# Optimization experiments

Hardware: AMD Instinct MI355X
Metric: run time of the kernel (lower is better)

## Reference

```python
import jax, jax.numpy as jnp
import numpy as np

IN_DIM = 768
OUT_DIM = 4096
N_SK_ITER = 3
TARGET_TEMP = 0.06
PRED_TEMP = 0.12
PREFACTOR = 1.0
EXP_MAX = 50.0  # exp_max_values[float32]
SK_EPS = 1e-8
NORM_EPS = 1e-7


def setup_inputs() -> dict:
    key = jax.random.key(0)
    kx, kw = jax.random.split(key)
    x = jax.random.normal(kx, (16, 1024, IN_DIM), dtype=jnp.float32)
    # nn.Linear weight init: normal(std=1); bias zeros
    weight = jax.random.normal(kw, (OUT_DIM, IN_DIM), dtype=jnp.float32)
    bias = jnp.zeros((OUT_DIM,), dtype=jnp.float32)
    return {"x": x, "weight": weight, "bias": bias}


def sinkhorn_knopp(M, n_iterations, eps=SK_EPS):
    # stable_exp: shift by max over dim=-2 (token axis), add EXP_MAX
    shift = jnp.max(M, axis=-2, keepdims=True)
    M = jnp.exp(M + EXP_MAX - shift)
    for _ in range(n_iterations):  # small fixed count
        M = M / (jnp.sum(M, axis=-2, keepdims=True) + eps)  # column normalize
        M = M / (jnp.sum(M, axis=-1, keepdims=True) + eps)  # row normalize
    return M


def reference(x, weight, bias):
    # L2 normalize features (eps matches torch F.normalize with p=2)
    norm = jnp.maximum(jnp.linalg.norm(x, axis=-1, keepdims=True), NORM_EPS)
    x_n = x / norm
    logits = jnp.einsum("bnd,kd->bnk", x_n, weight) + bias  # [B, N, K]
    # positionwise_sk=True: no flatten before sinkhorn; detach -> stop_gradient
    assignments = sinkhorn_knopp(jax.lax.stop_gradient(logits) / TARGET_TEMP, N_SK_ITER)
    tgt = assignments.reshape(-1, OUT_DIM).astype(jnp.float32)
    pred = logits.reshape(-1, OUT_DIM).astype(jnp.float32)
    loss = -jnp.mean(jnp.sum(tgt * jax.nn.log_softmax(pred / PRED_TEMP, axis=-1), axis=-1))
    return assignments, PREFACTOR * loss
```

## Files before the change

kernel.cpp:

```cpp
#include <hip/hip_runtime.h>
#include <math.h>

#define BATCH 16
#define NTOK  1024
#define NCLU  4096
#define DIM   768
#define MROWS (BATCH * NTOK)

constexpr float TT_INV    = 16.666666666666668f;
constexpr float PT_INV    = 8.333333333333334f;
constexpr float SK_EPS_   = 1e-8f;
constexpr float NORM_EPS_ = 1e-7f;
constexpr float COL_SHIFT = 60.0f;
constexpr float P_SHIFT   = 40.0f;

typedef _Float16 f16x8 __attribute__((ext_vector_type(8)));
typedef _Float16 f16x4 __attribute__((ext_vector_type(4)));
typedef float    f32x4 __attribute__((ext_vector_type(4)));

struct F8 { float v[8]; };

__device__ __forceinline__ F8 load8(const float* p) {
    const float4 a = *(const float4*)p;
    const float4 b = *(const float4*)(p + 4);
    return F8{{a.x, a.y, a.z, a.w, b.x, b.y, b.z, b.w}};
}
__device__ __forceinline__ F8 load8(const _Float16* p) {
    f16x8 h = *(const f16x8*)p;
    F8 r;
#pragma unroll
    for (int i = 0; i < 8; ++i) r.v[i] = (float)h[i];
    return r;
}

__device__ __forceinline__ float wave_sum(float s) {
#pragma unroll
    for (int off = 32; off; off >>= 1) s += __shfl_xor(s, off);
    return s;
}

__device__ __forceinline__ void gl_lds16(const void* g, void* l) {
    __builtin_amdgcn_global_load_lds(
        (const __attribute__((address_space(1))) unsigned int*)g,
        (__attribute__((address_space(3))) unsigned int*)l,
        16, 0, 0);
}

__global__ __launch_bounds__(256) void castx_kernel(
    const float* __restrict__ x, _Float16* __restrict__ x16)
{
    int row  = (blockIdx.x * 256 + threadIdx.x) >> 6;
    int lane = threadIdx.x & 63;
    const float4* rp = (const float4*)(x + (size_t)row * DIM);
    float4 v[3];
    float ss = 0.f;
#pragma unroll
    for (int i = 0; i < 3; ++i) {
        v[i] = rp[lane + i * 64];
        ss += v[i].x * v[i].x + v[i].y * v[i].y + v[i].z * v[i].z + v[i].w * v[i].w;
    }
    ss = wave_sum(ss);
    float sc = 1.0f / fmaxf(sqrtf(ss), NORM_EPS_);
    _Float16* op = x16 + (size_t)row * DIM;
#pragma unroll
    for (int i = 0; i < 3; ++i) {
        f16x4 h;
        h[0] = (_Float16)(v[i].x * sc); h[1] = (_Float16)(v[i].y * sc);
        h[2] = (_Float16)(v[i].z * sc); h[3] = (_Float16)(v[i].w * sc);
        *(f16x4*)(op + 4 * (lane + i * 64)) = h;
    }
}

__global__ __launch_bounds__(256) void castw_kernel(
    const float* __restrict__ w, _Float16* __restrict__ w16)
{
    int i = blockIdx.x * 256 + threadIdx.x;
    const float4 a = *(const float4*)(w + (size_t)i * 8);
    const float4 b = *(const float4*)(w + (size_t)i * 8 + 4);
    f16x8 h;
    h[0] = (_Float16)a.x; h[1] = (_Float16)a.y; h[2] = (_Float16)a.z; h[3] = (_Float16)a.w;
    h[4] = (_Float16)b.x; h[5] = (_Float16)b.y; h[6] = (_Float16)b.z; h[7] = (_Float16)b.w;
    *(f16x8*)(w16 + (size_t)i * 8) = h;
}

__global__ __launch_bounds__(256) void rownorm_kernel(
    const float* __restrict__ x, float* __restrict__ invn)
{
    int wave = (blockIdx.x * 256 + threadIdx.x) >> 6;
    int lane = threadIdx.x & 63;
    const float4* row = (const float4*)(x + (size_t)wave * DIM);
    float s = 0.f;
#pragma unroll
    for (int i = 0; i < 3; ++i) {
        float4 v = row[lane + i * 64];
        s += v.x * v.x + v.y * v.y + v.z * v.z + v.w * v.w;
    }
    s = wave_sum(s);
    if (lane == 0) invn[wave] = 1.0f / fmaxf(sqrtf(s), NORM_EPS_);
}

#define BM 128
#define BN 128
#define BK 32

__global__ __launch_bounds__(256) void gemm16(
    const _Float16* __restrict__ A,
    const _Float16* __restrict__ B,
    const float* __restrict__ bias,
    _Float16* __restrict__ out,
    float* __restrict__ colpart)
{
    __shared__ __align__(16) _Float16 sh[2 * BM * BK];
    _Float16* As = sh;
    _Float16* Bs = sh + BM * BK;

    const int tid  = threadIdx.x;
    const int lane = tid & 63;
    const int wid  = tid >> 6;
    const int wr = wid >> 1, wc = wid & 1;

    const int nwg = gridDim.x;
    const int cpx = nwg >> 3;
    const int bid = blockIdx.x;
    const int swz = (bid & 7) * cpx + (bid >> 3);
    const int brow = (swz >> 5) * BM;
    const int bcol = (swz & 31) * BN;

    const int r  = lane >> 2;
    const int s4 = lane & 3;
    const int srcslot = s4 ^ (r & 3) ^ (r >> 2);
    const int c0 = wid * 2, c1 = wid * 2 + 1;

    const _Float16* gA0 = A + (size_t)(brow + c0 * 16 + r) * DIM + srcslot * 8;
    const _Float16* gA1 = A + (size_t)(brow + c1 * 16 + r) * DIM + srcslot * 8;
    const _Float16* gB0 = B + (size_t)(bcol + c0 * 16 + r) * DIM + srcslot * 8;
    const _Float16* gB1 = B + (size_t)(bcol + c1 * 16 + r) * DIM + srcslot * 8;
    _Float16* lA0 = &As[c0 * 16 * BK];
    _Float16* lA1 = &As[c1 * 16 * BK];
    _Float16* lB0 = &Bs[c0 * 16 * BK];
    _Float16* lB1 = &Bs[c1 * 16 * BK];

    const int q  = lane >> 4;
    const int fr = lane & 15;
    const int slot = q ^ (fr & 3) ^ ((fr >> 2) & 3);
    const int aoff = (wr * 64 + fr) * BK + slot * 8;
    const int boff = (wc * 64 + fr) * BK + slot * 8;

    f32x4 acc[4][4] = {};

    const int NT = DIM / BK;
    for (int kt = 0; kt < NT; ++kt) {
        const int ko = kt * BK;
        __syncthreads();
        gl_lds16(gA0 + ko, lA0);
        gl_lds16(gA1 + ko, lA1);
        gl_lds16(gB0 + ko, lB0);
        gl_lds16(gB1 + ko, lB1);
        __syncthreads();

        f16x8 af[4], bf[4];
#pragma unroll
        for (int m = 0; m < 4; ++m)
            af[m] = *(const f16x8*)&As[aoff + m * 16 * BK];
#pragma unroll
        for (int n = 0; n < 4; ++n)
            bf[n] = *(const f16x8*)&Bs[boff + n * 16 * BK];
#pragma unroll
        for (int m = 0; m < 4; ++m)
#pragma unroll
            for (int n = 0; n < 4; ++n)
                acc[m][n] = __builtin_amdgcn_mfma_f32_16x16x32_f16(
                    af[m], bf[n], acc[m][n], 0, 0, 0);
    }

    float cs[4] = {0.f, 0.f, 0.f, 0.f};
    _Float16* Ct = sh;
#pragma unroll
    for (int h = 0; h < 2; ++h) {
        __syncthreads();
        if (wr == h) {
#pragma unroll
            for (int n = 0; n < 4; ++n) {
                const int coll = wc * 64 + n * 16 + fr;
                const float bv = bias[bcol + coll];
#pragma unroll
                for (int m = 0; m < 4; ++m) {
#pragma unroll
                    for (int j = 0; j < 4; ++j) {
                        float v = acc[m][n][j] + bv;
                        Ct[(m * 16 + (q << 2) + j) * BN + coll] = (_Float16)v;
                        cs[n] += __expf(v * TT_INV - COL_SHIFT);
                    }
                }
            }
        }
        __syncthreads();
#pragma unroll
        for (int i = 0; i < 4; ++i) {
            int c   = tid + i * 256;
            int rl  = c >> 4;
            int c16 = c & 15;
            f16x8 v = *(const f16x8*)&Ct[rl * BN + c16 * 8];
            *(f16x8*)(out + (size_t)(brow + h * 64 + rl) * NCLU + bcol + c16 * 8) = v;
        }
    }

    __syncthreads();
    float* cred = (float*)sh;
#pragma unroll
    for (int n = 0; n < 4; ++n) {
        float c2 = cs[n];
        c2 += __shfl_xor(c2, 16);
        c2 += __shfl_xor(c2, 32);
        if (q == 0) cred[((wr * 2 + wc) * 4 + n) * 16 + fr] = c2;
    }
    __syncthreads();
    if (tid < 128) {
        int wc2 = tid >> 6, n2 = (tid >> 4) & 3, fr2 = tid & 15;
        float S = cred[((0 * 2 + wc2) * 4 + n2) * 16 + fr2]
                + cred[((1 * 2 + wc2) * 4 + n2) * 16 + fr2];
        colpart[(size_t)(brow >> 7) * NCLU + bcol + wc2 * 64 + n2 * 16 + fr2] = S;
    }
}

__global__ __launch_bounds__(256) void colfin_kernel(
    const float* __restrict__ part, float* __restrict__ a1)
{
    int i = blockIdx.x * 256 + threadIdx.x;
    int b = i >> 12, k = i & (NCLU - 1);
    const float* p = part + (size_t)(b * 8) * NCLU + k;
    float s = 0.f;
#pragma unroll
    for (int rb = 0; rb < 8; ++rb) { s += *p; p += NCLU; }
    a1[i] = -COL_SHIFT - __logf(s);
}

#define LDK 40

__device__ __forceinline__ f16x8 pack8(float4 lo, float4 hi, float sc) {
    f16x8 h;
    h[0] = (_Float16)(lo.x * sc); h[1] = (_Float16)(lo.y * sc);
    h[2] = (_Float16)(lo.z * sc); h[3] = (_Float16)(lo.w * sc);
    h[4] = (_Float16)(hi.x * sc); h[5] = (_Float16)(hi.y * sc);
    h[6] = (_Float16)(hi.z * sc); h[7] = (_Float16)(hi.w * sc);
    return h;
}

template <typename OT>
__global__ __launch_bounds__(256) void gemm_f16(
    const float* __restrict__ x, const float* __restrict__ w,
    const float* __restrict__ bias, const float* __restrict__ invn,
    OT* __restrict__ out)
{
    __shared__ __align__(16) _Float16 As[BM * LDK];
    __shared__ __align__(16) _Float16 Bs[BN * LDK];

    const int tid  = threadIdx.x;
    const int lane = tid & 63;
    const int wid  = tid >> 6;
    const int wr = wid >> 1, wc = wid & 1;
    const int brow = blockIdx.y * BM;
    const int bcol = blockIdx.x * BN;

    const int r0 = tid >> 2;
    const int r1 = r0 + 64;
    const int kc = (tid & 3) * 8;
    const float sA0 = invn[brow + r0];
    const float sA1 = invn[brow + r1];
    const float* gA0 = x + (size_t)(brow + r0) * DIM + kc;
    const float* gA1 = x + (size_t)(brow + r1) * DIM + kc;
    const float* gB0 = w + (size_t)(bcol + r0) * DIM + kc;
    const float* gB1 = w + (size_t)(bcol + r1) * DIM + kc;

    f32x4 acc[4][4] = {};
    float4 a00, a01, a10, a11, b00, b01, b10, b11;
    a00 = *(const float4*)(gA0);     a01 = *(const float4*)(gA0 + 4);
    a10 = *(const float4*)(gA1);     a11 = *(const float4*)(gA1 + 4);
    b00 = *(const float4*)(gB0);     b01 = *(const float4*)(gB0 + 4);
    b10 = *(const float4*)(gB1);     b11 = *(const float4*)(gB1 + 4);

    const int NT = DIM / BK;
    for (int kt = 0; kt < NT; ++kt) {
        __syncthreads();
        *(f16x8*)&As[r0 * LDK + kc] = pack8(a00, a01, sA0);
        *(f16x8*)&As[r1 * LDK + kc] = pack8(a10, a11, sA1);
        *(f16x8*)&Bs[r0 * LDK + kc] = pack8(b00, b01, 1.0f);
        *(f16x8*)&Bs[r1 * LDK + kc] = pack8(b10, b11, 1.0f);
        __syncthreads();

        if (kt + 1 < NT) {
            int k0 = (kt + 1) * BK;
            a00 = *(const float4*)(gA0 + k0); a01 = *(const float4*)(gA0 + k0 + 4);
            a10 = *(const float4*)(gA1 + k0); a11 = *(const float4*)(gA1 + k0 + 4);
            b00 = *(const float4*)(gB0 + k0); b01 = *(const float4*)(gB0 + k0 + 4);
            b10 = *(const float4*)(gB1 + k0); b11 = *(const float4*)(gB1 + k0 + 4);
        }

        const int ko = (lane >> 4) * 8;
        f16x8 af[4], bf[4];
#pragma unroll
        for (int m = 0; m < 4; ++m)
            af[m] = *(const f16x8*)&As[(wr * 64 + m * 16 + (lane & 15)) * LDK + ko];
#pragma unroll
        for (int n = 0; n < 4; ++n)
            bf[n] = *(const f16x8*)&Bs[(wc * 64 + n * 16 + (lane & 15)) * LDK + ko];
#pragma unroll
        for (int m = 0; m < 4; ++m)
#pragma unroll
            for (int n = 0; n < 4; ++n)
                acc[m][n] = __builtin_amdgcn_mfma_f32_16x16x32_f16(
                    af[m], bf[n], acc[m][n], 0, 0, 0);
    }

#pragma unroll
    for (int n = 0; n < 4; ++n) {
        int col = bcol + wc * 64 + n * 16 + (lane & 15);
        float bv = bias[col];
#pragma unroll
        for (int m = 0; m < 4; ++m) {
            int row0 = brow + wr * 64 + m * 16 + ((lane >> 4) << 2);
#pragma unroll
            for (int j = 0; j < 4; ++j)
                out[(size_t)(row0 + j) * NCLU + col] = (OT)(acc[m][n][j] + bv);
        }
    }
}

template <typename T>
__global__ __launch_bounds__(256) void colpass_kernel(
    const T* __restrict__ L, const float* __restrict__ a_in,
    const float* __restrict__ b_in, float* __restrict__ a_out)
{
    __shared__ float bsh[NTOK];
    __shared__ float ss[4][64];
    int b = blockIdx.x >> 6;
    int k = ((blockIdx.x & 63) << 6) + (threadIdx.x & 63);
    int wv = threadIdx.x >> 6;
    int lane = threadIdx.x & 63;
    const bool first = (b_in == nullptr);
    if (first) {
        for (int i = threadIdx.x; i < NTOK; i += 256) bsh[i] = 0.f;
    } else {
        for (int i = threadIdx.x; i < NTOK; i += 256) bsh[i] = b_in[b * NTOK + i];
    }
    __syncthreads();
    float aval = first ? -COL_SHIFT : a_in[b * NCLU + k];
    const T* p = L + (size_t)b * NTOK * NCLU + (size_t)(wv * 256) * NCLU + k;
    float s = 0.f;
#pragma unroll 4
    for (int n = 0; n < 256; ++n) {
        s += __expf((float)(*p) * TT_INV + aval + bsh[wv * 256 + n]);
        p += NCLU;
    }
    ss[wv][lane] = s;
    __syncthreads();
    if (wv == 0) {
        float S = ss[0][lane] + ss[1][lane] + ss[2][lane] + ss[3][lane];
        a_out[b * NCLU + k] = aval - __logf(first ? S : S + SK_EPS_);
    }
}

template <typename T>
__global__ __launch_bounds__(256) void colpassV_kernel(
    const T* __restrict__ L, const float* __restrict__ a_in,
    const float* __restrict__ b_in, float* __restrict__ a_out)
{
    __shared__ float bsh[NTOK];
    __shared__ float red[16][16][8];
    const int b     = blockIdx.x >> 5;
    const int strip = blockIdx.x & 31;
    const int cc    = threadIdx.x & 15;
    const int rg    = threadIdx.x >> 4;
    const int col0  = strip * 128 + cc * 8;
    for (int i = threadIdx.x; i < NTOK; i += 256) bsh[i] = b_in[b * NTOK + i];
    __syncthreads();
    const float4 av0 = *(const float4*)(a_in + b * NCLU + col0);
    const float4 av1 = *(const float4*)(a_in + b * NCLU + col0 + 4);
    const float av[8] = {av0.x, av0.y, av0.z, av0.w, av1.x, av1.y, av1.z, av1.w};
    float s[8] = {};
    const T* p = L + (size_t)b * NTOK * NCLU + (size_t)rg * NCLU + col0;
    for (int it = 0; it < 64; ++it) {
        F8 Lv = load8(p);
        float bpv = bsh[it * 16 + rg];
#pragma unroll
        for (int j = 0; j < 8; ++j) s[j] += __expf(Lv.v[j] * TT_INV + av[j] + bpv);
        p += (size_t)16 * NCLU;
    }
#pragma unroll
    for (int j = 0; j < 8; ++j) red[rg][cc][j] = s[j];
    __syncthreads();
    if (threadIdx.x < 128) {
        int c2 = threadIdx.x >> 3, j2 = threadIdx.x & 7;
        float S = 0.f;
#pragma unroll
        for (int g = 0; g < 16; ++g) S += red[g][c2][j2];
        int col = strip * 128 + c2 * 8 + j2;
        a_out[b * NCLU + col] = a_in[b * NCLU + col] - __logf(S + SK_EPS_);
    }
}

template <typename T>
__global__ __launch_bounds__(256) void rowpass_kernel(
    const T* __restrict__ L, const float* __restrict__ a_in,
    const float* __restrict__ b_in, float* __restrict__ b_out)
{
    int row  = (blockIdx.x * 256 + threadIdx.x) >> 6;
    int lane = threadIdx.x & 63;
    int b = row >> 10;
    const T* Lr = L + (size_t)row * NCLU;
    const float* av = a_in + (size_t)b * NCLU;
    float bp = b_in ? b_in[row] : 0.f;
    float s = 0.f;
#pragma unroll
    for (int i = 0; i < 8; ++i) {
        int c = i * 64 + lane;
        F8 Lv = load8(Lr + c * 8);
        F8 Av = load8(av + c * 8);
#pragma unroll
        for (int j = 0; j < 8; ++j)
            s += __expf(Lv.v[j] * TT_INV + Av.v[j] + bp);
    }
    s = wave_sum(s);
    if (lane == 0) b_out[row] = bp - __logf(s + SK_EPS_);
}

template <typename T>
__global__ __launch_bounds__(256) void final_kernel(
    const T* __restrict__ L, const float* __restrict__ a3,
    const float* __restrict__ b2, float* __restrict__ out,
    float* __restrict__ rowloss)
{
    __shared__ float red[3][4];
    const int row  = blockIdx.x;
    const int tid  = threadIdx.x;
    const int lane = tid & 63;
    const int wv   = tid >> 6;
    const int b    = row >> 10;
    const T* Lr = L + (size_t)row * NCLU;
    const float* av = a3 + (size_t)b * NCLU;
    const float bp = b2[row];

    float e[2][8];
    float rs = 0.f, q = 0.f, sP = 0.f;
#pragma unroll
    for (int jj = 0; jj < 2; ++jj) {
        int c = tid + jj * 256;
        F8 Lv = load8(Lr + c * 8);
        F8 Av = load8(av + c * 8);
#pragma unroll
        for (int j = 0; j < 8; ++j) {
            float P  = Lv.v[j] * PT_INV;
            float ev = __expf(Lv.v[j] * TT_INV + Av.v[j] + bp);
            e[jj][j] = ev;
            rs += ev;
            q  += ev * P;
            sP += __expf(P - P_SHIFT);
        }
    }
    rs = wave_sum(rs); q = wave_sum(q); sP = wave_sum(sP);
    if (lane == 0) { red[0][wv] = rs; red[1][wv] = q; red[2][wv] = sP; }
    __syncthreads();
    rs = red[0][0] + red[0][1] + red[0][2] + red[0][3];
    q  = red[1][0] + red[1][1] + red[1][2] + red[1][3];
    sP = red[2][0] + red[2][1] + red[2][2] + red[2][3];

    const float inv = 1.0f / (rs + SK_EPS_);
    const float lse = P_SHIFT + __logf(sP);

    float* Or = out + (size_t)row * NCLU;
#pragma unroll
    for (int jj = 0; jj < 2; ++jj) {
        int c = tid + jj * 256;
        f32x4 w0, w1;
        w0[0] = e[jj][0] * inv; w0[1] = e[jj][1] * inv;
        w0[2] = e[jj][2] * inv; w0[3] = e[jj][3] * inv;
        w1[0] = e[jj][4] * inv; w1[1] = e[jj][5] * inv;
        w1[2] = e[jj][6] * inv; w1[3] = e[jj][7] * inv;
        __builtin_nontemporal_store(w0, (f32x4*)(Or + c * 8));
        __builtin_nontemporal_store(w1, (f32x4*)(Or + c * 8 + 4));
    }
    if (tid == 0) rowloss[row] = q * inv - lse * (rs * inv);
}

__global__ __launch_bounds__(256) void lossred_kernel(
    const float* __restrict__ rowloss, float* __restrict__ out_loss)
{
    __shared__ float red[4];
    int tid = threadIdx.x, lane = tid & 63, wv = tid >> 6;
    float s = 0.f;
    for (int i = tid; i < MROWS; i += 256) s += rowloss[i];
    s = wave_sum(s);
    if (lane == 0) red[wv] = s;
    __syncthreads();
    if (tid == 0)
        out_loss[0] = -(red[0] + red[1] + red[2] + red[3]) / (float)MROWS;
}

extern "C" void kernel_launch(void* const* d_in, const int* in_sizes, int n_in,
                              void* d_out, int out_size, void* d_ws, size_t ws_size,
                              hipStream_t stream)
{
    const float* x    = (const float*)d_in[0];
    const float* w    = (const float*)d_in[1];
    const float* bias = (const float*)d_in[2];
    float* out = (float*)d_out;
    char* base = (char*)d_ws;
    float* ws  = (float*)d_ws;

    float* a1      = ws;
    float* a2      = a1 + BATCH * NCLU;
    float* a3      = a2 + BATCH * NCLU;
    float* b1      = a3 + BATCH * NCLU;
    float* b2      = b1 + MROWS;
    float* rowloss = b2 + MROWS;

    const size_t SMALL = 1u << 20;
    const size_t L16B  = (size_t)MROWS * NCLU * 2;
    const size_t X16B  = (size_t)MROWS * DIM * 2;
    const size_t W16B  = (size_t)NCLU * DIM * 2;
    const size_t PARTB = (size_t)128 * NCLU * 4;

    const int CB = BATCH * (NCLU / 64);
    const int RB = MROWS / 4;

    if (ws_size >= SMALL + L16B + X16B + W16B + PARTB) {
        _Float16* L16 = (_Float16*)(base + SMALL);
        _Float16* X16 = (_Float16*)(base + SMALL + L16B);
        _Float16* W16 = (_Float16*)(base + SMALL + L16B + X16B);
        float*    part = (float*)(base + SMALL + L16B + X16B + W16B);
        castx_kernel<<<MROWS / 4, 256, 0, stream>>>(x, X16);
        castw_kernel<<<(NCLU * DIM / 8) / 256, 256, 0, stream>>>(w, W16);
        gemm16<<<(MROWS / BM) * (NCLU / BN), 256, 0, stream>>>(X16, W16, bias, L16, part);
        colfin_kernel<<<BATCH * NCLU / 256, 256, 0, stream>>>(part, a1);
        rowpass_kernel<_Float16><<<RB, 256, 0, stream>>>(L16, a1, nullptr, b1);
        colpassV_kernel<_Float16><<<BATCH * 32, 256, 0, stream>>>(L16, a1, b1, a2);
        rowpass_kernel<_Float16><<<RB, 256, 0, stream>>>(L16, a2, b1, b2);
        colpassV_kernel<_Float16><<<BATCH * 32, 256, 0, stream>>>(L16, a2, b2, a3);
        final_kernel<_Float16><<<MROWS, 256, 0, stream>>>(L16, a3, b2, out, rowloss);
        lossred_kernel<<<1, 256, 0, stream>>>(rowloss, out + (size_t)MROWS * NCLU);
    } else if (ws_size >= SMALL + L16B) {
        float* invn = rowloss + MROWS;
        _Float16* L16 = (_Float16*)(base + SMALL);
        rownorm_kernel<<<MROWS / 4, 256, 0, stream>>>(x, invn);
        dim3 gg(NCLU / BN, MROWS / BM);
        gemm_f16<_Float16><<<gg, 256, 0, stream>>>(x, w, bias, invn, L16);
        colpass_kernel<_Float16><<<CB, 256, 0, stream>>>(L16, nullptr, nullptr, a1);
        rowpass_kernel<_Float16><<<RB, 256, 0, stream>>>(L16, a1, nullptr, b1);
        colpassV_kernel<_Float16><<<BATCH * 32, 256, 0, stream>>>(L16, a1, b1, a2);
        rowpass_kernel<_Float16><<<RB, 256, 0, stream>>>(L16, a2, b1, b2);
        colpassV_kernel<_Float16><<<BATCH * 32, 256, 0, stream>>>(L16, a2, b2, a3);
        final_kernel<_Float16><<<MROWS, 256, 0, stream>>>(L16, a3, b2, out, rowloss);
        lossred_kernel<<<1, 256, 0, stream>>>(rowloss, out + (size_t)MROWS * NCLU);
    } else {
        float* invn = rowloss + MROWS;
        rownorm_kernel<<<MROWS / 4, 256, 0, stream>>>(x, invn);
        dim3 gg(NCLU / BN, MROWS / BM);
        gemm_f16<float><<<gg, 256, 0, stream>>>(x, w, bias, invn, out);
        colpass_kernel<float><<<CB, 256, 0, stream>>>(out, nullptr, nullptr, a1);
        rowpass_kernel<float><<<RB, 256, 0, stream>>>(out, a1, nullptr, b1);
        colpassV_kernel<float><<<BATCH * 32, 256, 0, stream>>>(out, a1, b1, a2);
        rowpass_kernel<float><<<RB, 256, 0, stream>>>(out, a2, b1, b2);
        colpassV_kernel<float><<<BATCH * 32, 256, 0, stream>>>(out, a2, b2, a3);
        final_kernel<float><<<MROWS, 256, 0, stream>>>(out, a3, b2, out, rowloss);
        lossred_kernel<<<1, 256, 0, stream>>>(rowloss, out + (size_t)MROWS * NCLU);
    }
}
```

Measured before the change: 375.8 us.

## Fuse Sinkhorn row and column passes into a single chunked kernel

Adds a kernel that, for each 16-row chunk, computes the row normalizers and then builds per-chunk column partial sums weighted by those normalizers. A small reduction kernel then finalizes the column scalings. This replaces the separate rowpass and colpassV launches and aims to cut full passes over the half-precision logits; the scratch space reuses the now-dead X16 region. The GEMM epilogue also drops its LDS-staged vectorized stores in favour of direct scattered 2-byte global stores, which saves barriers but may hurt write coalescing.

```diff
diff --git a/kernel.cpp b/kernel.cpp
--- a/kernel.cpp
+++ b/kernel.cpp
@@ -110,9 +110,8 @@
     _Float16* __restrict__ out,
     float* __restrict__ colpart)
 {
-    __shared__ __align__(16) _Float16 sh[2 * BM * BK];
-    _Float16* As = sh;
-    _Float16* Bs = sh + BM * BK;
+    __shared__ __align__(16) _Float16 As[BM * BK];
+    __shared__ __align__(16) _Float16 Bs[BN * BK];
 
     const int tid  = threadIdx.x;
     const int lane = tid & 63;
@@ -174,39 +173,23 @@
     }
 
     float cs[4] = {0.f, 0.f, 0.f, 0.f};
-    _Float16* Ct = sh;
-#pragma unroll
-    for (int h = 0; h < 2; ++h) {
-        __syncthreads();
-        if (wr == h) {
-#pragma unroll
-            for (int n = 0; n < 4; ++n) {
-                const int coll = wc * 64 + n * 16 + fr;
-                const float bv = bias[bcol + coll];
-#pragma unroll
-                for (int m = 0; m < 4; ++m) {
-#pragma unroll
-                    for (int j = 0; j < 4; ++j) {
-                        float v = acc[m][n][j] + bv;
-                        Ct[(m * 16 + (q << 2) + j) * BN + coll] = (_Float16)v;
-                        cs[n] += __expf(v * TT_INV - COL_SHIFT);
-                    }
-                }
+#pragma unroll
+    for (int n = 0; n < 4; ++n) {
+        int col = bcol + wc * 64 + n * 16 + fr;
+        float bv = bias[col];
+#pragma unroll
+        for (int m = 0; m < 4; ++m) {
+            int row0 = brow + wr * 64 + m * 16 + (q << 2);
+#pragma unroll
+            for (int j = 0; j < 4; ++j) {
+                float v = acc[m][n][j] + bv;
+                out[(size_t)(row0 + j) * NCLU + col] = (_Float16)v;
+                cs[n] += __expf(v * TT_INV - COL_SHIFT);
             }
         }
-        __syncthreads();
-#pragma unroll
-        for (int i = 0; i < 4; ++i) {
-            int c   = tid + i * 256;
-            int rl  = c >> 4;
-            int c16 = c & 15;
-            f16x8 v = *(const f16x8*)&Ct[rl * BN + c16 * 8];
-            *(f16x8*)(out + (size_t)(brow + h * 64 + rl) * NCLU + bcol + c16 * 8) = v;
-        }
-    }
-
-    __syncthreads();
-    float* cred = (float*)sh;
+    }
+    __syncthreads();
+    float* cred = (float*)&As[0];
 #pragma unroll
     for (int n = 0; n < 4; ++n) {
         float c2 = cs[n];
@@ -233,6 +216,94 @@
 #pragma unroll
     for (int rb = 0; rb < 8; ++rb) { s += *p; p += NCLU; }
     a1[i] = -COL_SHIFT - __logf(s);
+}
+
+template <bool FIRST>
+__global__ __launch_bounds__(256) void rcpass_kernel(
+    const _Float16* __restrict__ L, const float* __restrict__ a_in,
+    const float* __restrict__ b_in, float* __restrict__ b_out,
+    float* __restrict__ part)
+{
+    __shared__ float wgt_sh[16];
+    const int tid  = threadIdx.x;
+    const int lane = tid & 63;
+    const int wv   = tid >> 6;
+    const int chunk = blockIdx.x;
+    const int b     = chunk >> 6;
+    const int row0  = chunk * 16;
+    const float* av = a_in + (size_t)b * NCLU;
+
+    float ar[8][8];
+#pragma unroll
+    for (int i = 0; i < 8; ++i) {
+        int c = i * 64 + lane;
+        *(float4*)&ar[i][0] = *(const float4*)&av[c * 8];
+        *(float4*)&ar[i][4] = *(const float4*)&av[c * 8 + 4];
+    }
+
+#pragma unroll
+    for (int rr = 0; rr < 4; ++rr) {
+        int row = row0 + wv * 4 + rr;
+        const _Float16* Lr = L + (size_t)row * NCLU;
+        float bp = FIRST ? 0.f : b_in[row];
+        float s = 0.f;
+#pragma unroll
+        for (int i = 0; i < 8; ++i) {
+            int c = i * 64 + lane;
+            f16x8 h = *(const f16x8*)&Lr[c * 8];
+#pragma unroll
+            for (int j = 0; j < 8; ++j)
+                s += __expf((float)h[j] * TT_INV + ar[i][j] + bp);
+        }
+        s = wave_sum(s);
+        if (lane == 0) {
+            float bn = bp - __logf(s + SK_EPS_);
+            b_out[row] = bn;
+            wgt_sh[wv * 4 + rr] = __expf(bn);
+        }
+    }
+    __syncthreads();
+
+    float aown[2][8];
+#pragma unroll
+    for (int sl = 0; sl < 2; ++sl) {
+        *(float4*)&aown[sl][0] = *(const float4*)&av[sl * 2048 + tid * 8];
+        *(float4*)&aown[sl][4] = *(const float4*)&av[sl * 2048 + tid * 8 + 4];
+    }
+    float acc[2][8] = {};
+    for (int rr = 0; rr < 16; ++rr) {
+        const _Float16* Lr = L + (size_t)(row0 + rr) * NCLU;
+        float wg = wgt_sh[rr];
+#pragma unroll
+        for (int sl = 0; sl < 2; ++sl) {
+            f16x8 h = *(const f16x8*)&Lr[sl * 2048 + tid * 8];
+#pragma unroll
+            for (int j = 0; j < 8; ++j)
+                acc[sl][j] += __expf((float)h[j] * TT_INV + aown[sl][j]) * wg;
+        }
+    }
+    float* P = part + (size_t)chunk * NCLU;
+#pragma unroll
+    for (int sl = 0; sl < 2; ++sl) {
+        f32x4 w0, w1;
+        w0[0] = acc[sl][0]; w0[1] = acc[sl][1]; w0[2] = acc[sl][2]; w0[3] = acc[sl][3];
+        w1[0] = acc[sl][4]; w1[1] = acc[sl][5]; w1[2] = acc[sl][6]; w1[3] = acc[sl][7];
+        *(f32x4*)&P[sl * 2048 + tid * 8]     = w0;
+        *(f32x4*)&P[sl * 2048 + tid * 8 + 4] = w1;
+    }
+}
+
+__global__ __launch_bounds__(256) void colfinN_kernel(
+    const float* __restrict__ part, const float* __restrict__ a_in,
+    float* __restrict__ a_out)
+{
+    int i = blockIdx.x * 256 + threadIdx.x;
+    int b = i >> 12, k = i & (NCLU - 1);
+    const float* p = part + (size_t)(b * 64) * NCLU + k;
+    float s = 0.f;
+#pragma unroll 8
+    for (int c = 0; c < 64; ++c) { s += *p; p += NCLU; }
+    a_out[i] = a_in[i] - __logf(s + SK_EPS_);
 }
 
 #define LDK 40
@@ -527,15 +598,17 @@
         _Float16* L16 = (_Float16*)(base + SMALL);
         _Float16* X16 = (_Float16*)(base + SMALL + L16B);
         _Float16* W16 = (_Float16*)(base + SMALL + L16B + X16B);
-        float*    part = (float*)(base + SMALL + L16B + X16B + W16B);
+        float*    part1 = (float*)(base + SMALL + L16B + X16B + W16B);
+        float*    part  = (float*)(base + SMALL + L16B);
+
         castx_kernel<<<MROWS / 4, 256, 0, stream>>>(x, X16);
         castw_kernel<<<(NCLU * DIM / 8) / 256, 256, 0, stream>>>(w, W16);
-        gemm16<<<(MROWS / BM) * (NCLU / BN), 256, 0, stream>>>(X16, W16, bias, L16, part);
-        colfin_kernel<<<BATCH * NCLU / 256, 256, 0, stream>>>(part, a1);
-        rowpass_kernel<_Float16><<<RB, 256, 0, stream>>>(L16, a1, nullptr, b1);
-        colpassV_kernel<_Float16><<<BATCH * 32, 256, 0, stream>>>(L16, a1, b1, a2);
-        rowpass_kernel<_Float16><<<RB, 256, 0, stream>>>(L16, a2, b1, b2);
-        colpassV_kernel<_Float16><<<BATCH * 32, 256, 0, stream>>>(L16, a2, b2, a3);
+        gemm16<<<(MROWS / BM) * (NCLU / BN), 256, 0, stream>>>(X16, W16, bias, L16, part1);
+        colfin_kernel<<<BATCH * NCLU / 256, 256, 0, stream>>>(part1, a1);
+        rcpass_kernel<true ><<<MROWS / 16, 256, 0, stream>>>(L16, a1, nullptr, b1, part);
+        colfinN_kernel<<<BATCH * NCLU / 256, 256, 0, stream>>>(part, a1, a2);
+        rcpass_kernel<false><<<MROWS / 16, 256, 0, stream>>>(L16, a2, b1, b2, part);
+        colfinN_kernel<<<BATCH * NCLU / 256, 256, 0, stream>>>(part, a2, a3);
         final_kernel<_Float16><<<MROWS, 256, 0, stream>>>(L16, a3, b2, out, rowloss);
         lossred_kernel<<<1, 256, 0, stream>>>(rowloss, out + (size_t)MROWS * NCLU);
     } else if (ws_size >= SMALL + L16B) {
```

Result: faster. 353.9 us (-5.8%).
